# Optimization experiments

Hardware: AMD Instinct MI355X
Metric: run time of the kernel (lower is better)

The kernel has to match this reference:

```python
import jax, jax.numpy as jnp
import numpy as np

IMAGE = 800.0
HIGH_THRESH = 0.7   # torchvision RPN fg_iou_thresh
LOW_THRESH = 0.3    # torchvision RPN bg_iou_thresh
BELOW_LOW = -1      # Matcher.BELOW_LOW_THRESHOLD
BETWEEN = -2        # Matcher.BETWEEN_THRESHOLDS


def _make_boxes(key, shape, max_wh):
    # shape = (..., 4) target; build valid xyxy boxes inside the image
    k1, k2 = jax.random.split(key)
    xy = jax.random.uniform(k1, shape[:-1] + (2,)) * (IMAGE - max_wh)
    wh = jax.random.uniform(k2, shape[:-1] + (2,)) * (max_wh - 4.0) + 4.0
    return jnp.concatenate([xy, xy + wh], axis=-1)


def setup_inputs() -> dict:
    key = jax.random.key(0)
    kA, kG, kS, kC = jax.random.split(key, 4)
    B, A, G = 4, 160000, 64
    anchors = _make_boxes(kA, (B, A, 4), 128.0)
    gt_boxes = _make_boxes(kG, (B, G, 4), 200.0)
    # soft score labels in {0, 0.5, 1} style: mostly 1, some <1 (ignored), some 0
    u = jax.random.uniform(kS, (B, G))
    score_labels = jnp.where(u < 0.15, 0.0, jnp.where(u < 0.3, 0.5, 1.0)).astype(jnp.float32)
    confidence_labels = jax.random.randint(kC, (B, G), 0, 2).astype(jnp.int32)
    return {"anchors": anchors, "gt_boxes": gt_boxes,
            "score_labels": score_labels, "confidence_labels": confidence_labels}


def _box_iou(a, b):
    # a: [G,4] gt, b: [A,4] anchors -> [G,A]
    area_a = (a[:, 2] - a[:, 0]) * (a[:, 3] - a[:, 1])          # [G]
    area_b = (b[:, 2] - b[:, 0]) * (b[:, 3] - b[:, 1])          # [A]
    lt = jnp.maximum(a[:, None, :2], b[None, :, :2])            # [G,A,2]
    rb = jnp.minimum(a[:, None, 2:], b[None, :, 2:])            # [G,A,2]
    wh = jnp.clip(rb - lt, 0.0)
    inter = wh[..., 0] * wh[..., 1]                              # [G,A]
    return inter / (area_a[:, None] + area_b[None, :] - inter)


def _matcher(mq):
    # torchvision Matcher with allow_low_quality_matches=True. mq: [G,A]
    matched_vals = mq.max(axis=0)                                # [A]
    matches = mq.argmax(axis=0).astype(jnp.int32)                # [A]
    m = jnp.where(matched_vals < LOW_THRESH, BELOW_LOW,
                  jnp.where(matched_vals < HIGH_THRESH, BETWEEN, matches))
    # restore, for each gt, anchors achieving that gt's max IoU
    highest_per_gt = mq.max(axis=1, keepdims=True)               # [G,1]
    low_quality = (mq == highest_per_gt).any(axis=0)             # [A]
    return jnp.where(low_quality, matches, m)


def _assign_one(anchors, gt, scores, confs):
    mq = _box_iou(gt, anchors)                                   # [G,A]
    midx = _matcher(mq)                                          # [A]
    cl = jnp.clip(midx, 0)
    matched_gt = gt[cl]                                          # [A,4]
    pos = midx >= 0
    labels = pos.astype(jnp.float32)
    labels = jnp.minimum(labels, scores[cl])
    labels = jnp.where(midx == BELOW_LOW, 0.0, labels)
    labels = jnp.where(midx == BETWEEN, -1.0, labels)
    labels = jnp.where((scores[cl] < 1.0) & pos, -1.0, labels)
    labels = jnp.where((confs[cl] == 0) & pos, -1.0, labels)
    return labels, matched_gt


def reference(anchors, gt_boxes, score_labels, confidence_labels):
    labels, matched_gt_boxes = jax.vmap(_assign_one)(anchors, gt_boxes, score_labels, confidence_labels)
    return labels, matched_gt_boxes
```

## Files before the change

### kernel.cpp

```cpp
#include <hip/hip_runtime.h>

constexpr int NB = 4;
constexpr int NA = 160000;
constexpr int NG = 64;

__device__ __forceinline__ float box_area(float x0, float y0, float x1, float y1) {
#pragma clang fp contract(off)
    return (x1 - x0) * (y1 - y0);
}

__device__ __forceinline__ void inter_denom(float gx0, float gy0, float gx1, float gy1, float garea,
                                            float ax0, float ay0, float ax1, float ay1, float aarea,
                                            float& inter, float& denom) {
#pragma clang fp contract(off)
    float ltx = fmaxf(gx0, ax0);
    float lty = fmaxf(gy0, ay0);
    float rbx = fminf(gx1, ax1);
    float rby = fminf(gy1, ay1);
    float w = fmaxf(rbx - ltx, 0.0f);
    float h = fmaxf(rby - lty, 0.0f);
    inter = w * h;
    float s = garea + aarea;
    denom = s - inter;
}

__device__ __forceinline__ float iou_f(float gx0, float gy0, float gx1, float gy1, float garea,
                                       float ax0, float ay0, float ax1, float ay1, float aarea) {
    float inter, denom;
    inter_denom(gx0, gy0, gx1, gy1, garea, ax0, ay0, ax1, ay1, aarea, inter, denom);
    return inter / denom;
}

__device__ __forceinline__ bool frac_gt(float i1, float d1, float i2, float d2) {
    return (double)i1 * (double)d2 > (double)i2 * (double)d1;
}

__global__ __launch_bounds__(256) void k_gt_highest(
        const float* __restrict__ anchors, const float* __restrict__ gts,
        float* __restrict__ highest ) {
    const int b = blockIdx.y;
    const int lane = threadIdx.x & 63;
    const int wid = __builtin_amdgcn_readfirstlane(threadIdx.x >> 6);

    const float4* __restrict__ gt4 = reinterpret_cast<const float4*>(gts) + b * NG;
    const float4* __restrict__ anc = reinterpret_cast<const float4*>(anchors) + (size_t)b * NA;

    float4 g = gt4[lane];
    float garea = box_area(g.x, g.y, g.z, g.w);

    const int base = blockIdx.x * 160 + wid * 40;
    float bi = 0.0f, bd = 1.0f;
#pragma unroll 8
    for (int i = 0; i < 40; ++i) {
        float4 a = anc[base + i];
        float aarea = box_area(a.x, a.y, a.z, a.w);
        float inter, denom;
        inter_denom(g.x, g.y, g.z, g.w, garea, a.x, a.y, a.z, a.w, aarea,
                    inter, denom);
        if (frac_gt(inter, denom, bi, bd)) { bi = inter; bd = denom; }
    }

    __shared__ float pi[4][NG], pd[4][NG];
    pi[wid][lane] = bi;
    pd[wid][lane] = bd;
    __syncthreads();
    if (threadIdx.x < NG) {
        float ci = pi[0][threadIdx.x], cd = pd[0][threadIdx.x];
#pragma unroll
        for (int wv = 1; wv < 4; ++wv) {
            float ni = pi[wv][threadIdx.x], nd = pd[wv][threadIdx.x];
            if (frac_gt(ni, nd, ci, cd)) { ci = ni; cd = nd; }
        }
        float m = ci / cd;
        atomicMax(reinterpret_cast<int*>(&highest[b * NG + threadIdx.x]),
                  __float_as_int(m));
    }
}

__global__ __launch_bounds__(256) void k_assign(
        const float* __restrict__ anchors, const float* __restrict__ gts,
        const float* __restrict__ scores, const int* __restrict__ confs,
        const float* __restrict__ highest,
        float* __restrict__ labels_out, float4* __restrict__ boxes_out) {
    __shared__ float4 sg[NG];
    __shared__ float2 sah[NG];
    __shared__ float ssc[NG];
    __shared__ int scf[NG];

    const int b = blockIdx.y;
    if (threadIdx.x < NG) {
        const int gi = threadIdx.x;
        float4 gv = reinterpret_cast<const float4*>(gts)[b * NG + gi];
        sg[gi] = gv;
        sah[gi] = make_float2(box_area(gv.x, gv.y, gv.z, gv.w),
                              highest[b * NG + gi]);
        ssc[gi] = scores[b * NG + gi];
        scf[gi] = confs[b * NG + gi];
    }
    __syncthreads();

    const int ai = blockIdx.x * 256 + threadIdx.x;
    const float4* __restrict__ anc = reinterpret_cast<const float4*>(anchors) + (size_t)b * NA;
    float4 av = anc[ai];
    float aarea = box_area(av.x, av.y, av.z, av.w);

    float best = -1.0f;
    int   matches = 0;
    bool  lowq = false;
#pragma unroll 4
    for (int g = 0; g < NG; ++g) {
        float4 gb = sg[g];
        float2 ah = sah[g];
        float v = iou_f(gb.x, gb.y, gb.z, gb.w, ah.x,
                        av.x, av.y, av.z, av.w, aarea);
        if (v > best) { best = v; matches = g; }
        lowq |= (v == ah.y);
    }

    int m    = (best < 0.3f) ? -1 : ((best < 0.7f) ? -2 : matches);
    int midx = lowq ? matches : m;
    int cl   = (midx < 0) ? 0 : midx;

    float4 mg = sg[cl];
    float  sc = ssc[cl];
    int    cf = scf[cl];

    bool pos = (midx >= 0);
    float lab = pos ? 1.0f : 0.0f;
    lab = fminf(lab, sc);
    if (midx == -1) lab = 0.0f;
    if (midx == -2) lab = -1.0f;
    if (sc < 1.0f && pos) lab = -1.0f;
    if (cf == 0 && pos) lab = -1.0f;

    labels_out[(size_t)b * NA + ai] = lab;
    boxes_out[(size_t)b * NA + ai] = mg;
}

extern "C" void kernel_launch(void* const* d_in, const int* in_sizes, int n_in,
                              void* d_out, int out_size, void* d_ws, size_t ws_size,
                              hipStream_t stream) {
    const float* anchors = (const float*)d_in[0];
    const float* gts     = (const float*)d_in[1];
    const float* scores  = (const float*)d_in[2];
    const int*   confs   = (const int*)d_in[3];

    float* labels_out = (float*)d_out;
    float4* boxes_out = (float4*)((float*)d_out + (size_t)NB * NA);
    float* highest = (float*)d_ws;

    hipMemsetAsync(d_ws, 0, (size_t)NB * NG * sizeof(float), stream);

    dim3 g1(1000, NB), g2(625, NB), blk(256);
    k_gt_highest<<<g1, blk, 0, stream>>>(anchors, gts, highest);
    k_assign<<<g2, blk, 0, stream>>>(anchors, gts, scores, confs, highest,
                                     labels_out, boxes_out);
}
```

Measured before the change: 142.7 us.

## Precompute GT metadata in workspace and read it via uniform scalar loads

The first kernel now packs each GT box, its area, score and confidence into a workspace table. The assign kernel's inner loop reads that table and the per-GT highest IoU directly from global memory at wave-uniform addresses, so the compiler can use scalar loads instead of LDS reads. The GT-max kernel also splits its reduction into four independent accumulators to increase instruction-level parallelism. The cost is more scalar loads and register pressure in the assign loop, plus a cross-kernel dependency on the workspace layout.

```diff
diff --git a/kernel.cpp b/kernel.cpp
--- a/kernel.cpp
+++ b/kernel.cpp
@@ -3,6 +3,7 @@
 constexpr int NB = 4;
 constexpr int NA = 160000;
 constexpr int NG = 64;
+
 
 __device__ __forceinline__ float box_area(float x0, float y0, float x1, float y1) {
 #pragma clang fp contract(off)
@@ -37,7 +38,8 @@
 
 __global__ __launch_bounds__(256) void k_gt_highest(
         const float* __restrict__ anchors, const float* __restrict__ gts,
-        float* __restrict__ highest ) {
+        const float* __restrict__ scores, const int* __restrict__ confs,
+        float* __restrict__ ws) {
     const int b = blockIdx.y;
     const int lane = threadIdx.x & 63;
     const int wid = __builtin_amdgcn_readfirstlane(threadIdx.x >> 6);
@@ -49,20 +51,35 @@
     float garea = box_area(g.x, g.y, g.z, g.w);
 
     const int base = blockIdx.x * 160 + wid * 40;
-    float bi = 0.0f, bd = 1.0f;
-#pragma unroll 8
-    for (int i = 0; i < 40; ++i) {
-        float4 a = anc[base + i];
-        float aarea = box_area(a.x, a.y, a.z, a.w);
-        float inter, denom;
-        inter_denom(g.x, g.y, g.z, g.w, garea, a.x, a.y, a.z, a.w, aarea,
-                    inter, denom);
-        if (frac_gt(inter, denom, bi, bd)) { bi = inter; bd = denom; }
+    float bi0 = 0.0f, bd0 = 1.0f, bi1 = 0.0f, bd1 = 1.0f;
+    float bi2 = 0.0f, bd2 = 1.0f, bi3 = 0.0f, bd3 = 1.0f;
+#pragma unroll
+    for (int i = 0; i < 40; i += 4) {
+        float4 a0 = anc[base + i];
+        float4 a1 = anc[base + i + 1];
+        float4 a2 = anc[base + i + 2];
+        float4 a3 = anc[base + i + 3];
+        float in0, dn0, in1, dn1, in2, dn2, in3, dn3;
+        inter_denom(g.x, g.y, g.z, g.w, garea, a0.x, a0.y, a0.z, a0.w,
+                    box_area(a0.x, a0.y, a0.z, a0.w), in0, dn0);
+        inter_denom(g.x, g.y, g.z, g.w, garea, a1.x, a1.y, a1.z, a1.w,
+                    box_area(a1.x, a1.y, a1.z, a1.w), in1, dn1);
+        inter_denom(g.x, g.y, g.z, g.w, garea, a2.x, a2.y, a2.z, a2.w,
+                    box_area(a2.x, a2.y, a2.z, a2.w), in2, dn2);
+        inter_denom(g.x, g.y, g.z, g.w, garea, a3.x, a3.y, a3.z, a3.w,
+                    box_area(a3.x, a3.y, a3.z, a3.w), in3, dn3);
+        if (frac_gt(in0, dn0, bi0, bd0)) { bi0 = in0; bd0 = dn0; }
+        if (frac_gt(in1, dn1, bi1, bd1)) { bi1 = in1; bd1 = dn1; }
+        if (frac_gt(in2, dn2, bi2, bd2)) { bi2 = in2; bd2 = dn2; }
+        if (frac_gt(in3, dn3, bi3, bd3)) { bi3 = in3; bd3 = dn3; }
     }
+    if (frac_gt(bi1, bd1, bi0, bd0)) { bi0 = bi1; bd0 = bd1; }
+    if (frac_gt(bi3, bd3, bi2, bd2)) { bi2 = bi3; bd2 = bd3; }
+    if (frac_gt(bi2, bd2, bi0, bd0)) { bi0 = bi2; bd0 = bd2; }
 
     __shared__ float pi[4][NG], pd[4][NG];
-    pi[wid][lane] = bi;
-    pd[wid][lane] = bd;
+    pi[wid][lane] = bi0;
+    pd[wid][lane] = bd0;
     __syncthreads();
     if (threadIdx.x < NG) {
         float ci = pi[0][threadIdx.x], cd = pd[0][threadIdx.x];
@@ -72,30 +89,38 @@
             if (frac_gt(ni, nd, ci, cd)) { ci = ni; cd = nd; }
         }
         float m = ci / cd;
-        atomicMax(reinterpret_cast<int*>(&highest[b * NG + threadIdx.x]),
+        atomicMax(reinterpret_cast<int*>(&ws[b * NG + threadIdx.x]),
                   __float_as_int(m));
+    }
+
+    if (blockIdx.x == 0 && threadIdx.x < NG) {
+        const int gi = threadIdx.x;
+        float4 gv = gt4[gi];
+        float ga = box_area(gv.x, gv.y, gv.z, gv.w);
+        float4* meta4 = reinterpret_cast<float4*>(ws + NB * NG) + (b * NG + gi) * 2;
+        meta4[0] = gv;
+        meta4[1] = make_float4(ga, 0.0f, scores[b * NG + gi],
+                               __int_as_float(confs[b * NG + gi]));
     }
 }
 
 __global__ __launch_bounds__(256) void k_assign(
-        const float* __restrict__ anchors, const float* __restrict__ gts,
-        const float* __restrict__ scores, const int* __restrict__ confs,
-        const float* __restrict__ highest,
+        const float* __restrict__ anchors, const float* __restrict__ ws,
         float* __restrict__ labels_out, float4* __restrict__ boxes_out) {
-    __shared__ float4 sg[NG];
-    __shared__ float2 sah[NG];
+    const int b = blockIdx.y;
+    const float* __restrict__ hi = ws + b * NG;
+    const float4* __restrict__ meta4 =
+        reinterpret_cast<const float4*>(ws + NB * NG) + (size_t)b * NG * 2;
+
+    __shared__ float4 sbox[NG];
     __shared__ float ssc[NG];
     __shared__ int scf[NG];
-
-    const int b = blockIdx.y;
     if (threadIdx.x < NG) {
-        const int gi = threadIdx.x;
-        float4 gv = reinterpret_cast<const float4*>(gts)[b * NG + gi];
-        sg[gi] = gv;
-        sah[gi] = make_float2(box_area(gv.x, gv.y, gv.z, gv.w),
-                              highest[b * NG + gi]);
-        ssc[gi] = scores[b * NG + gi];
-        scf[gi] = confs[b * NG + gi];
+        float4 mA = meta4[threadIdx.x * 2];
+        float4 mB = meta4[threadIdx.x * 2 + 1];
+        sbox[threadIdx.x] = mA;
+        ssc[threadIdx.x] = mB.z;
+        scf[threadIdx.x] = __float_as_int(mB.w);
     }
     __syncthreads();
 
@@ -107,21 +132,22 @@
     float best = -1.0f;
     int   matches = 0;
     bool  lowq = false;
-#pragma unroll 4
+#pragma unroll 8
     for (int g = 0; g < NG; ++g) {
-        float4 gb = sg[g];
-        float2 ah = sah[g];
-        float v = iou_f(gb.x, gb.y, gb.z, gb.w, ah.x,
+        float4 mA = meta4[g * 2];
+        float4 mB = meta4[g * 2 + 1];
+        float hg = hi[g];
+        float v = iou_f(mA.x, mA.y, mA.z, mA.w, mB.x,
                         av.x, av.y, av.z, av.w, aarea);
         if (v > best) { best = v; matches = g; }
-        lowq |= (v == ah.y);
+        lowq |= (v == hg);
     }
 
     int m    = (best < 0.3f) ? -1 : ((best < 0.7f) ? -2 : matches);
     int midx = lowq ? matches : m;
     int cl   = (midx < 0) ? 0 : midx;
 
-    float4 mg = sg[cl];
+    float4 mg = sbox[cl];
     float  sc = ssc[cl];
     int    cf = scf[cl];
 
@@ -147,12 +173,11 @@
 
     float* labels_out = (float*)d_out;
     float4* boxes_out = (float4*)((float*)d_out + (size_t)NB * NA);
-    float* highest = (float*)d_ws;
+    float* ws = (float*)d_ws;
 
     hipMemsetAsync(d_ws, 0, (size_t)NB * NG * sizeof(float), stream);
 
     dim3 g1(1000, NB), g2(625, NB), blk(256);
-    k_gt_highest<<<g1, blk, 0, stream>>>(anchors, gts, highest);
-    k_assign<<<g2, blk, 0, stream>>>(anchors, gts, scores, confs, highest,
-                                     labels_out, boxes_out);
+    k_gt_highest<<<g1, blk, 0, stream>>>(anchors, gts, scores, confs, ws);
+    k_assign<<<g2, blk, 0, stream>>>(anchors, ws, labels_out, boxes_out);
 }
```

Result: slower. 145.8 us (+2.2%).

## Fuse max-IoU reduction and assignment into one cooperative kernel with grid sync

Applied to the files above, without the earlier changes.

Replaces the memset plus two kernel launches with a single cooperative kernel of 500 blocks. Each wave first computes per-gt partial max IoU over 320 anchors and writes it to workspace. After a grid-wide sync, every block redundantly reduces the 125 partials for its batch and then assigns 1280 anchors (5 per thread). This removes launch and memset overhead and the atomics, and amortizes the shared-memory gt loads over more anchors. The cost is a grid barrier, a redundant per-block reduction over workspace, and fewer blocks (500), which may underfill the GPU.

```diff
diff --git a/kernel.cpp b/kernel.cpp
--- a/kernel.cpp
+++ b/kernel.cpp
@@ -1,8 +1,14 @@
 #include <hip/hip_runtime.h>
+#include <hip/hip_cooperative_groups.h>
+
+namespace cg = cooperative_groups;
 
 constexpr int NB = 4;
 constexpr int NA = 160000;
 constexpr int NG = 64;
+constexpr int NBLK = 500;
+constexpr int NWAVE = NBLK * 4;
+
 
 __device__ __forceinline__ float box_area(float x0, float y0, float x1, float y1) {
 #pragma clang fp contract(off)
@@ -35,106 +41,134 @@
     return (double)i1 * (double)d2 > (double)i2 * (double)d1;
 }
 
-__global__ __launch_bounds__(256) void k_gt_highest(
+__global__ __launch_bounds__(256, 2) void k_fused(
         const float* __restrict__ anchors, const float* __restrict__ gts,
-        float* __restrict__ highest ) {
-    const int b = blockIdx.y;
-    const int lane = threadIdx.x & 63;
-    const int wid = __builtin_amdgcn_readfirstlane(threadIdx.x >> 6);
+        const float* __restrict__ scores, const int* __restrict__ confs,
+        float* __restrict__ ws,
+        float* __restrict__ labels_out, float4* __restrict__ boxes_out) {
+    const int tid = threadIdx.x;
+    const int lane = tid & 63;
+    const int wid = __builtin_amdgcn_readfirstlane(tid >> 6);
+    const int j = blockIdx.x;
 
-    const float4* __restrict__ gt4 = reinterpret_cast<const float4*>(gts) + b * NG;
-    const float4* __restrict__ anc = reinterpret_cast<const float4*>(anchors) + (size_t)b * NA;
+    float* __restrict__ pi = ws;
+    float* __restrict__ pd = ws + NWAVE * NG;
 
-    float4 g = gt4[lane];
-    float garea = box_area(g.x, g.y, g.z, g.w);
+    {
+        const int w = j * 4 + wid;
+        const int b1 = w / 500;
+        const int widx = w % 500;
+        const float4* __restrict__ gt4 = reinterpret_cast<const float4*>(gts) + b1 * NG;
+        const float4* __restrict__ anc = reinterpret_cast<const float4*>(anchors) + (size_t)b1 * NA;
 
-    const int base = blockIdx.x * 160 + wid * 40;
-    float bi = 0.0f, bd = 1.0f;
+        float4 g = gt4[lane];
+        float garea = box_area(g.x, g.y, g.z, g.w);
+
+        const int base = widx * 320;
+        float bi = 0.0f, bd = 1.0f;
 #pragma unroll 8
-    for (int i = 0; i < 40; ++i) {
-        float4 a = anc[base + i];
-        float aarea = box_area(a.x, a.y, a.z, a.w);
-        float inter, denom;
-        inter_denom(g.x, g.y, g.z, g.w, garea, a.x, a.y, a.z, a.w, aarea,
-                    inter, denom);
-        if (frac_gt(inter, denom, bi, bd)) { bi = inter; bd = denom; }
+        for (int i = 0; i < 320; ++i) {
+            float4 a = anc[base + i];
+            float aarea = box_area(a.x, a.y, a.z, a.w);
+            float in, dn;
+            inter_denom(g.x, g.y, g.z, g.w, garea, a.x, a.y, a.z, a.w, aarea, in, dn);
+            if (frac_gt(in, dn, bi, bd)) { bi = in; bd = dn; }
+        }
+        pi[w * NG + lane] = bi;
+        pd[w * NG + lane] = bd;
     }
 
-    __shared__ float pi[4][NG], pd[4][NG];
-    pi[wid][lane] = bi;
-    pd[wid][lane] = bd;
+    cg::this_grid().sync();
+
+    const int b = j & 3;
+    const int jb = j >> 2;
+
+    __shared__ float ri[4][NG], rd[4][NG];
+    __shared__ float4 sg[NG];
+    __shared__ float sga[NG], shi[NG], ssc[NG];
+    __shared__ int scf[NG];
+    {
+        const int w0 = b * 500 + wid * 125;
+        float ci = pi[(size_t)w0 * NG + lane], cd = pd[(size_t)w0 * NG + lane];
+#pragma unroll 4
+        for (int i = 1; i < 125; ++i) {
+            float ni = pi[(size_t)(w0 + i) * NG + lane];
+            float nd = pd[(size_t)(w0 + i) * NG + lane];
+            if (frac_gt(ni, nd, ci, cd)) { ci = ni; cd = nd; }
+        }
+        ri[wid][lane] = ci;
+        rd[wid][lane] = cd;
+    }
     __syncthreads();
-    if (threadIdx.x < NG) {
-        float ci = pi[0][threadIdx.x], cd = pd[0][threadIdx.x];
+    if (tid < NG) {
+        float ci = ri[0][tid], cd = rd[0][tid];
 #pragma unroll
         for (int wv = 1; wv < 4; ++wv) {
-            float ni = pi[wv][threadIdx.x], nd = pd[wv][threadIdx.x];
+            float ni = ri[wv][tid], nd = rd[wv][tid];
             if (frac_gt(ni, nd, ci, cd)) { ci = ni; cd = nd; }
         }
-        float m = ci / cd;
-        atomicMax(reinterpret_cast<int*>(&highest[b * NG + threadIdx.x]),
-                  __float_as_int(m));
-    }
-}
+        shi[tid] = ci / cd;
 
-__global__ __launch_bounds__(256) void k_assign(
-        const float* __restrict__ anchors, const float* __restrict__ gts,
-        const float* __restrict__ scores, const int* __restrict__ confs,
-        const float* __restrict__ highest,
-        float* __restrict__ labels_out, float4* __restrict__ boxes_out) {
-    __shared__ float4 sg[NG];
-    __shared__ float2 sah[NG];
-    __shared__ float ssc[NG];
-    __shared__ int scf[NG];
-
-    const int b = blockIdx.y;
-    if (threadIdx.x < NG) {
-        const int gi = threadIdx.x;
-        float4 gv = reinterpret_cast<const float4*>(gts)[b * NG + gi];
-        sg[gi] = gv;
-        sah[gi] = make_float2(box_area(gv.x, gv.y, gv.z, gv.w),
-                              highest[b * NG + gi]);
-        ssc[gi] = scores[b * NG + gi];
-        scf[gi] = confs[b * NG + gi];
+        float4 gv = reinterpret_cast<const float4*>(gts)[b * NG + tid];
+        sg[tid] = gv;
+        sga[tid] = box_area(gv.x, gv.y, gv.z, gv.w);
+        ssc[tid] = scores[b * NG + tid];
+        scf[tid] = confs[b * NG + tid];
     }
     __syncthreads();
 
-    const int ai = blockIdx.x * 256 + threadIdx.x;
     const float4* __restrict__ anc = reinterpret_cast<const float4*>(anchors) + (size_t)b * NA;
-    float4 av = anc[ai];
-    float aarea = box_area(av.x, av.y, av.z, av.w);
+    const int a0 = jb * 1280 + tid;
 
-    float best = -1.0f;
-    int   matches = 0;
-    bool  lowq = false;
-#pragma unroll 4
+    float4 av[5];
+    float aarea[5], best[5];
+    int matches[5];
+    bool lowq[5];
+#pragma unroll
+    for (int k = 0; k < 5; ++k) {
+        av[k] = anc[a0 + k * 256];
+        aarea[k] = box_area(av[k].x, av[k].y, av[k].z, av[k].w);
+        best[k] = -1.0f;
+        matches[k] = 0;
+        lowq[k] = false;
+    }
+
+#pragma unroll 2
     for (int g = 0; g < NG; ++g) {
         float4 gb = sg[g];
-        float2 ah = sah[g];
-        float v = iou_f(gb.x, gb.y, gb.z, gb.w, ah.x,
-                        av.x, av.y, av.z, av.w, aarea);
-        if (v > best) { best = v; matches = g; }
-        lowq |= (v == ah.y);
+        float ga = sga[g];
+        float hg = shi[g];
+#pragma unroll
+        for (int k = 0; k < 5; ++k) {
+            float v = iou_f(gb.x, gb.y, gb.z, gb.w, ga,
+                            av[k].x, av[k].y, av[k].z, av[k].w, aarea[k]);
+            if (v > best[k]) { best[k] = v; matches[k] = g; }
+            lowq[k] |= (v == hg);
+        }
     }
 
-    int m    = (best < 0.3f) ? -1 : ((best < 0.7f) ? -2 : matches);
-    int midx = lowq ? matches : m;
-    int cl   = (midx < 0) ? 0 : midx;
+    const size_t obase = (size_t)b * NA;
+#pragma unroll
+    for (int k = 0; k < 5; ++k) {
+        int m    = (best[k] < 0.3f) ? -1 : ((best[k] < 0.7f) ? -2 : matches[k]);
+        int midx = lowq[k] ? matches[k] : m;
+        int cl   = (midx < 0) ? 0 : midx;
 
-    float4 mg = sg[cl];
-    float  sc = ssc[cl];
-    int    cf = scf[cl];
+        float4 mg = sg[cl];
+        float  sc = ssc[cl];
+        int    cf = scf[cl];
 
-    bool pos = (midx >= 0);
-    float lab = pos ? 1.0f : 0.0f;
-    lab = fminf(lab, sc);
-    if (midx == -1) lab = 0.0f;
-    if (midx == -2) lab = -1.0f;
-    if (sc < 1.0f && pos) lab = -1.0f;
-    if (cf == 0 && pos) lab = -1.0f;
+        bool pos = (midx >= 0);
+        float lab = pos ? 1.0f : 0.0f;
+        lab = fminf(lab, sc);
+        if (midx == -1) lab = 0.0f;
+        if (midx == -2) lab = -1.0f;
+        if (sc < 1.0f && pos) lab = -1.0f;
+        if (cf == 0 && pos) lab = -1.0f;
 
-    labels_out[(size_t)b * NA + ai] = lab;
-    boxes_out[(size_t)b * NA + ai] = mg;
+        labels_out[obase + a0 + k * 256] = lab;
+        boxes_out[obase + a0 + k * 256] = mg;
+    }
 }
 
 extern "C" void kernel_launch(void* const* d_in, const int* in_sizes, int n_in,
@@ -147,12 +181,10 @@
 
     float* labels_out = (float*)d_out;
     float4* boxes_out = (float4*)((float*)d_out + (size_t)NB * NA);
-    float* highest = (float*)d_ws;
+    float* ws = (float*)d_ws;
 
-    hipMemsetAsync(d_ws, 0, (size_t)NB * NG * sizeof(float), stream);
-
-    dim3 g1(1000, NB), g2(625, NB), blk(256);
-    k_gt_highest<<<g1, blk, 0, stream>>>(anchors, gts, highest);
-    k_assign<<<g2, blk, 0, stream>>>(anchors, gts, scores, confs, highest,
-                                     labels_out, boxes_out);
+    void* args[] = {(void*)&anchors, (void*)&gts, (void*)&scores, (void*)&confs,
+                    (void*)&ws, (void*)&labels_out, (void*)&boxes_out};
+    hipLaunchCooperativeKernel((const void*)k_fused, dim3(NBLK), dim3(256),
+                               args, 0, stream);
 }
```

Result: slower. 205.4 us (+43.9%).
